# Kernel optimization log

Hardware: AMD Instinct MI355X
Metric: run time of the kernel (lower is better)

Reference implementation:

```python
import jax, jax.numpy as jnp
import numpy as np

GRID = (128, 128, 128)
CENTER = (0.0, 0.0, 0.0)
SIZE = (400.0, 400.0, 400.0)
KERNEL_WIDTH = float(np.sqrt(3.0 * 3.0 * np.pi))  # ~5.317 (from module source)
SIGMA = KERNEL_WIDTH / 2.0
W = 2  # transverse window half-width in voxels (kernel_width / voxel_size ~ 1.7)
ROTATIONS = {'x': [1, 2, 0], 'y': [0, 2, 1], 'z': [0, 1, 2]}
N_LORS = 200000


def _make_lors(key, n, axis, half):
    # endpoints: main-axis coords pinned to the two FOV faces, transverse uniform
    u = jax.random.uniform(key, (n, 6), minval=-half, maxval=half, dtype=jnp.float32)
    u = u.at[:, axis].set(-half).at[:, axis + 3].set(half)
    return u


def setup_inputs() -> dict:
    key = jax.random.key(0)
    k0, k1, k2, k3 = jax.random.split(key, 4)
    image = jax.random.uniform(k0, GRID, dtype=jnp.float32)
    half = SIZE[0] / 2.0
    return {
        'image': image,
        'xlors': _make_lors(k1, N_LORS, 0, half),
        'ylors': _make_lors(k2, N_LORS, 1, half),
        'zlors': _make_lors(k3, N_LORS, 2, half),
    }


def _project_axis(image, lors, perm):
    # rotate image / geometry so the LOR main axis is the last (slice) axis
    img = jnp.transpose(image, perm)                      # [gx, gy, gz]
    g = [GRID[i] for i in perm]
    c = [CENTER[i] for i in perm]
    s = [SIZE[i] for i in perm]
    dx, dy, dz = s[0] / g[0], s[1] / g[1], s[2] / g[2]
    xmin, ymin, zmin = c[0] - s[0] / 2, c[1] - s[1] / 2, c[2] - s[2] / 2

    p0 = lors[:, jnp.array(perm)]                          # [N,3]
    p1 = lors[:, jnp.array([i + 3 for i in perm])]         # [N,3]
    dvec = p1 - p0
    L = jnp.sqrt(jnp.sum(dvec * dvec, axis=1))             # LOR length
    dzl = dvec[:, 2]
    path = dz * L / jnp.abs(dzl)                           # path length per slice

    di = jnp.arange(-W, W + 1)
    doff = jnp.stack(jnp.meshgrid(di, di, indexing='ij'), -1).reshape(-1, 2)  # [25,2]

    def step(acc, k):
        zc = zmin + (k.astype(jnp.float32) + 0.5) * dz     # slice-plane center
        t = (zc - p0[:, 2]) / dzl                          # [N] line parameter
        xc = p0[:, 0] + t * dvec[:, 0]
        yc = p0[:, 1] + t * dvec[:, 1]
        i0 = jnp.floor((xc - xmin) / dx).astype(jnp.int32)
        j0 = jnp.floor((yc - ymin) / dy).astype(jnp.int32)
        ii = i0[:, None] + doff[None, :, 0]                # [N,25]
        jj = j0[:, None] + doff[None, :, 1]
        xi = xmin + (ii.astype(jnp.float32) + 0.5) * dx
        yj = ymin + (jj.astype(jnp.float32) + 0.5) * dy
        d2 = (xi - xc[:, None]) ** 2 + (yj - yc[:, None]) ** 2
        w = jnp.exp(-d2 / (2.0 * SIGMA * SIGMA))
        w = w * (d2 <= KERNEL_WIDTH * KERNEL_WIDTH).astype(jnp.float32)
        inb = ((ii >= 0) & (ii < g[0]) & (jj >= 0) & (jj < g[1])).astype(jnp.float32)
        valid = ((t >= 0.0) & (t <= 1.0)).astype(jnp.float32)
        sl = jax.lax.dynamic_index_in_dim(img, k, axis=2, keepdims=False)  # [gx,gy]
        vals = sl[jnp.clip(ii, 0, g[0] - 1), jnp.clip(jj, 0, g[1] - 1)]
        contrib = jnp.sum(w * inb * vals, axis=1) * path * valid
        return acc + contrib, None

    acc, _ = jax.lax.scan(step, jnp.zeros(lors.shape[0], jnp.float32), jnp.arange(g[2]))
    return acc


def reference(image, xlors, ylors, zlors):
    px = _project_axis(image, xlors, ROTATIONS['x'])
    py = _project_axis(image, ylors, ROTATIONS['y'])
    pz = _project_axis(image, zlors, ROTATIONS['z'])
    return jnp.stack([px, py, pz])  # [3, N]
```

## Files before the change

### kernel.cpp

```cpp
#include <hip/hip_runtime.h>
#include <math.h>

constexpr float DXC    = 3.125f;
constexpr float INV_DX = 0.32f;
constexpr float XMINC  = -200.0f;
constexpr float KW2    = 9.0f * 3.14159265358979323846f;
constexpr float DXC2   = DXC * DXC;
constexpr float KW2C   = KW2 / DXC2;
constexpr float NEGL2C = -(2.0f / KW2) * 1.4426950408889634f * DXC2;
constexpr float WOFF   = 1.7983f;

constexpr int TPB    = 1024;
constexpr int LPB    = 1024;
constexpr int KSPLIT = 4;
constexpr int KCH    = 128 / KSPLIT;
constexpr int QTAB   = 1024;

__device__ inline unsigned bf16_rn(float x) {
    unsigned u = __float_as_uint(x);
    return (u + 0x7fffu + ((u >> 16) & 1u)) >> 16;
}
__device__ inline unsigned pk_bf16(float x, float y) {
    return bf16_rn(x) | (bf16_rn(y) << 16);
}
__device__ inline float uaf(unsigned u) { return __uint_as_float(u); }

__global__ __launch_bounds__(256) void prep2_kernel(const float* __restrict__ img,
                                                    ushort* __restrict__ V0, ushort* __restrict__ V1,
                                                    ushort* __restrict__ V2, ushort* __restrict__ S0,
                                                    ushort* __restrict__ S1, ushort* __restrict__ S2) {
    int o = blockIdx.x * 256 + threadIdx.x;
    int c = o & 127, b = (o >> 7) & 127, a = o >> 14;
    float x  = img[o];
    float xn = (c < 127) ? img[o + 1] : 0.0f;
    unsigned h  = bf16_rn(x);
    unsigned hn = bf16_rn(xn);
    V0[o] = (ushort)h;
    S0[o] = (ushort)((c < 127) ? hn : 0u);
    int p1 = (b << 14) | (a << 7) | c;
    V1[p1] = (ushort)h;
    S1[p1] = (ushort)((c < 127) ? hn : 0u);
    V2[o] = (ushort)bf16_rn(img[(b << 14) | (c << 7) | a]);
    S2[o] = (ushort)((c < 127) ? bf16_rn(img[(b << 14) | ((c + 1) << 7) | a]) : 0u);
}

__global__ __launch_bounds__(256) void prep_kernel(const float* __restrict__ img,
                                                   ushort* __restrict__ V0,
                                                   ushort* __restrict__ V1,
                                                   ushort* __restrict__ V2) {
    int o = blockIdx.x * 256 + threadIdx.x;
    float x = img[o];
    unsigned h = bf16_rn(x);
    V0[o] = (ushort)h;
    int c = o & 127, b = (o >> 7) & 127, a = o >> 14;
    V1[(b << 14) | (a << 7) | c] = (ushort)h;
    int j = o & 127, i = (o >> 7) & 127, k = o >> 14;
    V2[o] = (ushort)bf16_rn(img[(i << 14) | (j << 7) | k]);
}

__global__ __launch_bounds__(1024) void zero_kernel(float* __restrict__ out, int m) {
    int i = blockIdx.x * 1024 + threadIdx.x;
    if (i < m) out[i] = 0.0f;
}

__device__ inline void stage_one(const ushort* __restrict__ V, int k, int tid, void* dst) {
    const char* src = (const char*)(V + ((size_t)k << 14));
    char* d = (char*)dst;
    int wbase = (tid >> 6) << 10;
    int lane16 = (tid & 63) << 4;
#pragma unroll
    for (int c = 0; c < 2; ++c) {
        int half = c << 14;
        __builtin_amdgcn_global_load_lds(
            (__attribute__((address_space(1))) void*)(const_cast<char*>(src + half + wbase + lane16)),
            (__attribute__((address_space(3))) void*)(d + half + wbase),
            16, 0, 0);
    }
}

struct WIN {
    float eb[4], ea[4], b[4], t[4];
    const uint* base;
    int adw;
};

__device__ inline WIN make_window(float u, float v, const uint2* wt,
                                  const uint* A, const uint* B) {
    WIN w;
    float e0f = fminf(fmaxf(floorf(v - WOFF), 0.0f), 124.0f);
    int   e0  = (int)e0f;
    int   qv  = min((int)((v - e0f) * (QTAB / 4.0f)), QTAB - 1);
    uint2 tb = wt[qv];
    w.eb[0] = uaf(tb.x << 16); w.eb[1] = uaf(tb.x & 0xffff0000u);
    w.eb[2] = uaf(tb.y << 16); w.eb[3] = uaf(tb.y & 0xffff0000u);
    float db0 = e0f + 0.5f - v;
    w.b[0] = db0 * db0;
    float gb = fmaf(2.0f, db0, 1.0f);
    w.b[1] = w.b[0] + gb; float gb1 = gb + 2.0f;
    w.b[2] = w.b[1] + gb1;
    w.b[3] = w.b[2] + gb1 + 2.0f;

    float i0f = fminf(fmaxf(floorf(u - WOFF), 0.0f), 124.0f);
    int   i0c = (int)i0f;
    int   qu  = min((int)((u - i0f) * (QTAB / 4.0f)), QTAB - 1);
    uint2 ta = wt[qu];
    w.ea[0] = uaf(ta.x << 16); w.ea[1] = uaf(ta.x & 0xffff0000u);
    w.ea[2] = uaf(ta.y << 16); w.ea[3] = uaf(ta.y & 0xffff0000u);
    float da0 = i0f + 0.5f - u;
    float a0 = da0 * da0;
    float ga = fmaf(2.0f, da0, 1.0f);
    float a1 = a0 + ga; float ga1 = ga + 2.0f;
    float a2 = a1 + ga1;
    float a3 = a2 + ga1 + 2.0f;
    w.t[0] = KW2C - a0; w.t[1] = KW2C - a1; w.t[2] = KW2C - a2; w.t[3] = KW2C - a3;

    w.base = (e0 & 1) ? B : A;
    w.adw  = (i0c << 6) + (e0 >> 1);
    return w;
}

template <int AXIS>
__device__ void proj_axis8(uint* slA, uint* slB, uint2* wt,
                           const ushort* __restrict__ V, const ushort* __restrict__ S,
                           const float* __restrict__ lors,
                           float* __restrict__ out, int n, int blk, int ks)
{
    const int tid = threadIdx.x;
    const int lor = blk * LPB + tid;
    const bool active = lor < n;
    const int lorc = active ? lor : n - 1;

    const float* l = lors + (size_t)lorc * 6;
    float l0 = l[0], l1 = l[1], l2 = l[2], l3 = l[3], l4 = l[4], l5 = l[5];
    float p0x, p0y, p0z, p1x, p1y, p1z;
    if (AXIS == 0)      { p0x = l1; p0y = l2; p0z = l0; p1x = l4; p1y = l5; p1z = l3; }
    else if (AXIS == 1) { p0x = l0; p0y = l2; p0z = l1; p1x = l3; p1y = l5; p1z = l4; }
    else                { p0x = l0; p0y = l1; p0z = l2; p1x = l3; p1y = l4; p1z = l5; }

    float dvx = p1x - p0x, dvy = p1y - p0y, dvz = p1z - p0z;
    float L     = sqrtf(dvx * dvx + dvy * dvy + dvz * dvz);
    float pathL = DXC * L / fabsf(dvz);
    float invdz = 1.0f / dvz;

    float dux  = dvx * INV_DX, ux0 = (p0x - XMINC) * INV_DX;
    float dvyS = dvy * INV_DX, vy0 = (p0y - XMINC) * INV_DX;
    float tzs = invdz, tz0 = -p0z * invdz;

    const int k0 = ks * KCH, k1 = k0 + KCH;
    float dt = DXC * tzs;
    float cu = dux * dt, cv = dvyS * dt;
    float zc0 = fmaf((float)k0, DXC, XMINC + 0.5f * DXC);
    float t0  = fmaf(zc0, tzs, tz0);
    float u   = fmaf(t0, dux, ux0);
    float v   = fmaf(t0, dvyS, vy0);
    float acc = 0.0f;

    stage_one(V, k0, tid, slA);
    stage_one(S, k0, tid, slB);
    {
        float s = ((float)tid + 0.5f) * (4.0f / (float)QTAB);
        float o0 = 0.5f - s, o1 = 1.5f - s, o2 = 2.5f - s, o3 = 3.5f - s;
        float e0 = exp2f(o0 * o0 * NEGL2C);
        float e1 = exp2f(o1 * o1 * NEGL2C);
        float e2 = exp2f(o2 * o2 * NEGL2C);
        float e3 = exp2f(o3 * o3 * NEGL2C);
        wt[tid] = make_uint2(pk_bf16(e0, e1), pk_bf16(e2, e3));
    }
    __syncthreads();

    WIN w = make_window(u, v, wt, slA, slB);

    for (int k = k0; k < k1; ++k) {
#pragma unroll
        for (int r = 0; r < 4; ++r) {
            uint d0 = w.base[w.adw + (r << 6)];
            uint d1 = w.base[w.adw + (r << 6) + 1];
            float w0 = uaf(d0 << 16);
            float w1 = uaf(d0 & 0xffff0000u);
            float w2 = uaf(d1 << 16);
            float w3 = uaf(d1 & 0xffff0000u);
            float tr = w.t[r];
            float rs;
            rs = __fmul_rn((w.b[0] <= tr) ? w.eb[0] : 0.0f, w0);
            rs = fmaf((w.b[1] <= tr) ? w.eb[1] : 0.0f, w1, rs);
            rs = fmaf((w.b[2] <= tr) ? w.eb[2] : 0.0f, w2, rs);
            rs = fmaf((w.b[3] <= tr) ? w.eb[3] : 0.0f, w3, rs);
            acc = fmaf(w.ea[r], rs, acc);
        }

        if (k < k1 - 1) {
            float un = u + cu, vn = v + cv;
            __syncthreads();
            stage_one(V, k + 1, tid, slA);
            stage_one(S, k + 1, tid, slB);
            w = make_window(un, vn, wt, slA, slB);
            u = un; v = vn;
            __syncthreads();
        }
    }

    if (active) atomicAdd(out + lor, acc * pathL);
}

__global__ __launch_bounds__(TPB, 8) void proj_fused8(const ushort* __restrict__ V0,
                                                      const ushort* __restrict__ V1,
                                                      const ushort* __restrict__ V2,
                                                      const ushort* __restrict__ S0,
                                                      const ushort* __restrict__ S1,
                                                      const ushort* __restrict__ S2,
                                                      const float* __restrict__ xl,
                                                      const float* __restrict__ yl,
                                                      const float* __restrict__ zl,
                                                      float* __restrict__ out,
                                                      int n, int nblk)
{
    __shared__ uint  slA[8192];
    __shared__ uint  slB[8192];
    __shared__ uint2 wt[QTAB];
    int per = nblk * KSPLIT;
    int axis = blockIdx.x / per;
    int r = blockIdx.x - axis * per;
    int blk = r >> 2;
    int ks  = r & 3;
    if (axis == 0)      proj_axis8<0>(slA, slB, wt, V0, S0, xl, out, n, blk, ks);
    else if (axis == 1) proj_axis8<1>(slA, slB, wt, V1, S1, yl, out + n, n, blk, ks);
    else                proj_axis8<2>(slA, slB, wt, V2, S2, zl, out + 2 * (size_t)n, n, blk, ks);
}

template <int AXIS>
__device__ inline void stage_issue(const float* __restrict__ img, int k, int tid,
                                   float4 st[4]) {
#pragma unroll
    for (int c = 0; c < 4; ++c) {
        int f4 = tid + TPB * c;
        int fl = f4 << 2;
        if (AXIS == 2) {
            int i = fl >> 7, j = fl & 127;
            const float* p = img + (i << 14) + (j << 7) + k;
            st[c] = make_float4(p[0], p[128], p[256], p[384]);
        } else {
            int off;
            if (AXIS == 1) off = ((fl >> 7) << 14) | (k << 7) | (fl & 127);
            else           off = (k << 14) | fl;
            st[c] = *reinterpret_cast<const float4*>(img + off);
        }
    }
}

__device__ inline void stage_write(const float4 st[4], ushort* slb, int tid) {
    uint* w = reinterpret_cast<uint*>(slb);
#pragma unroll
    for (int c = 0; c < 4; ++c) {
        int f4 = tid + TPB * c;
        w[f4 * 2]     = pk_bf16(st[c].x, st[c].y);
        w[f4 * 2 + 1] = pk_bf16(st[c].z, st[c].w);
    }
}

template <int AXIS, bool PRE>
__device__ void proj_axis7(ushort (*sl)[16384], float4* wtab,
                           const ushort* __restrict__ V,
                           const float*  __restrict__ imgF,
                           const float*  __restrict__ lors,
                           float* __restrict__ out, int n, int blk, int ks)
{
    const int tid = threadIdx.x;
    const int lor = blk * LPB + tid;
    const bool active = lor < n;
    const int lorc = active ? lor : n - 1;

    const float* l = lors + (size_t)lorc * 6;
    float l0 = l[0], l1 = l[1], l2 = l[2], l3 = l[3], l4 = l[4], l5 = l[5];
    float p0x, p0y, p0z, p1x, p1y, p1z;
    if (AXIS == 0)      { p0x = l1; p0y = l2; p0z = l0; p1x = l4; p1y = l5; p1z = l3; }
    else if (AXIS == 1) { p0x = l0; p0y = l2; p0z = l1; p1x = l3; p1y = l5; p1z = l4; }
    else                { p0x = l0; p0y = l1; p0z = l2; p1x = l3; p1y = l4; p1z = l5; }

    float dvx = p1x - p0x, dvy = p1y - p0y, dvz = p1z - p0z;
    float L     = sqrtf(dvx * dvx + dvy * dvy + dvz * dvz);
    float pathL = DXC * L / fabsf(dvz);
    float invdz = 1.0f / dvz;

    float dux  = dvx * INV_DX, ux0 = (p0x - XMINC) * INV_DX;
    float dvyS = dvy * INV_DX, vy0 = (p0y - XMINC) * INV_DX;
    float tzs = invdz, tz0 = -p0z * invdz;

    const int k0 = ks * KCH, k1 = k0 + KCH;
    float dt = DXC * tzs;
    float cu = dux * dt, cv = dvyS * dt;
    float zc0 = fmaf((float)k0, DXC, XMINC + 0.5f * DXC);
    float t0  = fmaf(zc0, tzs, tz0);
    float u   = fmaf(t0, dux, ux0);
    float v   = fmaf(t0, dvyS, vy0);
    float acc = 0.0f;

    if (PRE) {
        stage_one(V, k0, tid, sl[k0 & 1]);
    } else {
        float4 st[4];
        stage_issue<AXIS>(imgF, k0, tid, st);
        stage_write(st, sl[k0 & 1], tid);
    }
    {
        float s = ((float)tid + 0.5f) * (4.0f / (float)QTAB);
        float4 e;
        float o0 = 0.5f - s, o1 = 1.5f - s, o2 = 2.5f - s, o3 = 3.5f - s;
        e.x = exp2f(o0 * o0 * NEGL2C);
        e.y = exp2f(o1 * o1 * NEGL2C);
        e.z = exp2f(o2 * o2 * NEGL2C);
        e.w = exp2f(o3 * o3 * NEGL2C);
        wtab[tid] = e;
    }
    __syncthreads();

    for (int k = k0; k < k1; ++k) {
        const ushort* sbuf = sl[k & 1];
        float4 st2[4];
        if (k < k1 - 1) {
            if (PRE) stage_one(V, k + 1, tid, sl[(k & 1) ^ 1]);
            else     stage_issue<AXIS>(imgF, k + 1, tid, st2);
        }

        float e0f = fminf(fmaxf(floorf(v - WOFF), 0.0f), 124.0f);
        int   e0  = (int)e0f;
        int   qv  = min((int)((v - e0f) * (QTAB / 4.0f)), QTAB - 1);
        float4 eb = wtab[qv];
        float db0 = e0f + 0.5f - v;
        float b0 = db0 * db0;
        float gb = fmaf(2.0f, db0, 1.0f);
        float b1 = b0 + gb, gb1 = gb + 2.0f;
        float b2 = b1 + gb1, gb2 = gb1 + 2.0f;
        float b3 = b2 + gb2;

        float i0f = fminf(fmaxf(floorf(u - WOFF), 0.0f), 124.0f);
        int   i0c = (int)i0f;
        int   qu  = min((int)((u - i0f) * (QTAB / 4.0f)), QTAB - 1);
        float4 ea = wtab[qu];
        float da0 = i0f + 0.5f - u;
        float a0 = da0 * da0;
        float ga = fmaf(2.0f, da0, 1.0f);
        float a1 = a0 + ga, ga1 = ga + 2.0f;
        float a2 = a1 + ga1, ga2 = ga1 + 2.0f;
        float a3 = a2 + ga2;
        float thr[4] = {KW2C - a0, KW2C - a1, KW2C - a2, KW2C - a3};
        float eaa[4] = {ea.x, ea.y, ea.z, ea.w};

        const uint* s32 = reinterpret_cast<const uint*>(sbuf);
        int dwc = e0 >> 1;
        int sh  = (e0 & 1) << 4;
        int rowdw = (i0c << 6) + dwc;
#pragma unroll
        for (int r = 0; r < 4; ++r) {
            const uint* sr = s32 + rowdw + (r << 6);
            uint d0 = sr[0], d1 = sr[1], d2 = sr[2];
            uint p01 = __builtin_amdgcn_alignbit(d1, d0, sh);
            uint p23 = __builtin_amdgcn_alignbit(d2, d1, sh);
            float w0 = uaf(p01 << 16);
            float w1 = uaf(p01 & 0xffff0000u);
            float w2 = uaf(p23 << 16);
            float w3 = uaf(p23 & 0xffff0000u);
            float tr = thr[r];
            float rs;
            rs = __fmul_rn((b0 <= tr) ? eb.x : 0.0f, w0);
            rs = fmaf((b1 <= tr) ? eb.y : 0.0f, w1, rs);
            rs = fmaf((b2 <= tr) ? eb.z : 0.0f, w2, rs);
            rs = fmaf((b3 <= tr) ? eb.w : 0.0f, w3, rs);
            acc = fmaf(eaa[r], rs, acc);
        }

        u += cu; v += cv;

        if (k < k1 - 1) {
            if (!PRE) stage_write(st2, sl[(k & 1) ^ 1], tid);
            __syncthreads();
        }
    }

    if (active) atomicAdd(out + lor, acc * pathL);
}

template <bool PRE>
__global__ __launch_bounds__(TPB, 8) void proj_fused7(const float* __restrict__ img,
                                                      const ushort* __restrict__ V0,
                                                      const ushort* __restrict__ V1,
                                                      const ushort* __restrict__ V2,
                                                      const float* __restrict__ xl,
                                                      const float* __restrict__ yl,
                                                      const float* __restrict__ zl,
                                                      float* __restrict__ out,
                                                      int n, int nblk)
{
    __shared__ ushort sl[2][16384];
    __shared__ float4 wtab[QTAB];
    int per = nblk * KSPLIT;
    int axis = blockIdx.x / per;
    int r = blockIdx.x - axis * per;
    int blk = r >> 2;
    int ks  = r & 3;
    if (axis == 0)      proj_axis7<0, PRE>(sl, wtab, V0, img, xl, out, n, blk, ks);
    else if (axis == 1) proj_axis7<1, PRE>(sl, wtab, V1, img, yl, out + n, n, blk, ks);
    else                proj_axis7<2, PRE>(sl, wtab, V2, img, zl, out + 2 * (size_t)n, n, blk, ks);
}

extern "C" void kernel_launch(void* const* d_in, const int* in_sizes, int n_in,
                              void* d_out, int out_size, void* d_ws, size_t ws_size,
                              hipStream_t stream) {
    const float* img   = (const float*)d_in[0];
    const float* xlors = (const float*)d_in[1];
    const float* ylors = (const float*)d_in[2];
    const float* zlors = (const float*)d_in[3];
    float* out = (float*)d_out;

    int n = in_sizes[1] / 6;
    int nblk = (n + LPB - 1) / LPB;
    int m = 3 * n;

    zero_kernel<<<(m + 1023) / 1024, 1024, 0, stream>>>(out, m);

    constexpr size_t VOL = 128 * 128 * 128;
    int grid = 3 * nblk * KSPLIT;

    if (ws_size >= 6 * VOL * sizeof(ushort)) {
        ushort* V0 = (ushort*)d_ws;
        ushort* V1 = V0 + VOL;  ushort* V2 = V1 + VOL;
        ushort* S0 = V2 + VOL;  ushort* S1 = S0 + VOL;  ushort* S2 = S1 + VOL;
        prep2_kernel<<<VOL / 256, 256, 0, stream>>>(img, V0, V1, V2, S0, S1, S2);
        proj_fused8<<<grid, TPB, 0, stream>>>(V0, V1, V2, S0, S1, S2,
                                              xlors, ylors, zlors, out, n, nblk);
    } else if (ws_size >= 3 * VOL * sizeof(ushort)) {
        ushort* V0 = (ushort*)d_ws;
        ushort* V1 = V0 + VOL;  ushort* V2 = V1 + VOL;
        prep_kernel<<<VOL / 256, 256, 0, stream>>>(img, V0, V1, V2);
        proj_fused7<true><<<grid, TPB, 0, stream>>>(img, V0, V1, V2,
                                                    xlors, ylors, zlors, out, n, nblk);
    } else {
        proj_fused7<false><<<grid, TPB, 0, stream>>>(img, nullptr, nullptr, nullptr,
                                                     xlors, ylors, zlors, out, n, nblk);
    }
}
```

Before: 326.3 us.

## Process two LORs per thread per staged slice and replace the window mask with a weight threshold

```diff
diff --git a/kernel.cpp b/kernel.cpp
--- a/kernel.cpp
+++ b/kernel.cpp
@@ -9,10 +9,12 @@
 constexpr float KW2C   = KW2 / DXC2;
 constexpr float NEGL2C = -(2.0f / KW2) * 1.4426950408889634f * DXC2;
 constexpr float WOFF   = 1.7983f;
+constexpr float WMIN   = 0.13533528323661270f;
 
 constexpr int TPB    = 1024;
 constexpr int LPB    = 1024;
-constexpr int KSPLIT = 4;
+constexpr int LPT    = 2;
+constexpr int KSPLIT = 8;
 constexpr int KCH    = 128 / KSPLIT;
 constexpr int QTAB   = 1024;
 
@@ -78,131 +80,126 @@
     }
 }
 
-struct WIN {
-    float eb[4], ea[4], b[4], t[4];
-    const uint* base;
-    int adw;
-};
-
-__device__ inline WIN make_window(float u, float v, const uint2* wt,
-                                  const uint* A, const uint* B) {
-    WIN w;
-    float e0f = fminf(fmaxf(floorf(v - WOFF), 0.0f), 124.0f);
-    int   e0  = (int)e0f;
-    int   qv  = min((int)((v - e0f) * (QTAB / 4.0f)), QTAB - 1);
-    uint2 tb = wt[qv];
-    w.eb[0] = uaf(tb.x << 16); w.eb[1] = uaf(tb.x & 0xffff0000u);
-    w.eb[2] = uaf(tb.y << 16); w.eb[3] = uaf(tb.y & 0xffff0000u);
-    float db0 = e0f + 0.5f - v;
-    w.b[0] = db0 * db0;
-    float gb = fmaf(2.0f, db0, 1.0f);
-    w.b[1] = w.b[0] + gb; float gb1 = gb + 2.0f;
-    w.b[2] = w.b[1] + gb1;
-    w.b[3] = w.b[2] + gb1 + 2.0f;
-
-    float i0f = fminf(fmaxf(floorf(u - WOFF), 0.0f), 124.0f);
-    int   i0c = (int)i0f;
-    int   qu  = min((int)((u - i0f) * (QTAB / 4.0f)), QTAB - 1);
-    uint2 ta = wt[qu];
-    w.ea[0] = uaf(ta.x << 16); w.ea[1] = uaf(ta.x & 0xffff0000u);
-    w.ea[2] = uaf(ta.y << 16); w.ea[3] = uaf(ta.y & 0xffff0000u);
-    float da0 = i0f + 0.5f - u;
-    float a0 = da0 * da0;
-    float ga = fmaf(2.0f, da0, 1.0f);
-    float a1 = a0 + ga; float ga1 = ga + 2.0f;
-    float a2 = a1 + ga1;
-    float a3 = a2 + ga1 + 2.0f;
-    w.t[0] = KW2C - a0; w.t[1] = KW2C - a1; w.t[2] = KW2C - a2; w.t[3] = KW2C - a3;
-
-    w.base = (e0 & 1) ? B : A;
-    w.adw  = (i0c << 6) + (e0 >> 1);
-    return w;
-}
+struct WIN { float ea0, ea1, ea2, ea3, eb0, eb1, eb2, eb3; int adw; };
+struct LST { float u, v, cu, cv, path; };
 
 template <int AXIS>
-__device__ void proj_axis8(uint* slA, uint* slB, uint2* wt,
-                           const ushort* __restrict__ V, const ushort* __restrict__ S,
-                           const float* __restrict__ lors,
-                           float* __restrict__ out, int n, int blk, int ks)
-{
-    const int tid = threadIdx.x;
-    const int lor = blk * LPB + tid;
-    const bool active = lor < n;
-    const int lorc = active ? lor : n - 1;
-
+__device__ inline LST lor_setup(const float* __restrict__ lors, int lorc, int k0) {
     const float* l = lors + (size_t)lorc * 6;
     float l0 = l[0], l1 = l[1], l2 = l[2], l3 = l[3], l4 = l[4], l5 = l[5];
     float p0x, p0y, p0z, p1x, p1y, p1z;
     if (AXIS == 0)      { p0x = l1; p0y = l2; p0z = l0; p1x = l4; p1y = l5; p1z = l3; }
     else if (AXIS == 1) { p0x = l0; p0y = l2; p0z = l1; p1x = l3; p1y = l5; p1z = l4; }
     else                { p0x = l0; p0y = l1; p0z = l2; p1x = l3; p1y = l4; p1z = l5; }
-
     float dvx = p1x - p0x, dvy = p1y - p0y, dvz = p1z - p0z;
     float L     = sqrtf(dvx * dvx + dvy * dvy + dvz * dvz);
-    float pathL = DXC * L / fabsf(dvz);
     float invdz = 1.0f / dvz;
-
+    LST s;
+    s.path = DXC * L / fabsf(dvz);
     float dux  = dvx * INV_DX, ux0 = (p0x - XMINC) * INV_DX;
     float dvyS = dvy * INV_DX, vy0 = (p0y - XMINC) * INV_DX;
-    float tzs = invdz, tz0 = -p0z * invdz;
+    float tz0 = -p0z * invdz;
+    float dt = DXC * invdz;
+    s.cu = dux * dt; s.cv = dvyS * dt;
+    float zc0 = fmaf((float)k0, DXC, XMINC + 0.5f * DXC);
+    float t0  = fmaf(zc0, invdz, tz0);
+    s.u = fmaf(t0, dux, ux0);
+    s.v = fmaf(t0, dvyS, vy0);
+    return s;
+}
+
+__device__ inline WIN mkwin(float u, float v, const float4* wt) {
+    WIN w;
+    float e0f = fminf(fmaxf(floorf(v - WOFF), 0.0f), 124.0f);
+    float i0f = fminf(fmaxf(floorf(u - WOFF), 0.0f), 124.0f);
+    int qv = min((int)((v - e0f) * (QTAB / 4.0f)), QTAB - 1);
+    int qu = min((int)((u - i0f) * (QTAB / 4.0f)), QTAB - 1);
+    float4 eb = wt[qv];
+    float4 ea = wt[qu];
+    int e0 = (int)e0f, i0 = (int)i0f;
+    w.adw = (i0 << 6) + (e0 >> 1) + ((e0 & 1) << 13);
+    w.ea0 = ea.x; w.ea1 = ea.y; w.ea2 = ea.z; w.ea3 = ea.w;
+    w.eb0 = eb.x; w.eb1 = eb.y; w.eb2 = eb.z; w.eb3 = eb.w;
+    return w;
+}
+
+__device__ inline float do_slice(const WIN& w, const uint* __restrict__ sl, float acc) {
+#pragma unroll
+    for (int r = 0; r < 4; ++r) {
+        int a = w.adw + (r << 6);
+        uint d0 = sl[a], d1 = sl[a + 1];
+        float x0 = uaf(d0 << 16), x1 = uaf(d0 & 0xffff0000u);
+        float x2 = uaf(d1 << 16), x3 = uaf(d1 & 0xffff0000u);
+        float er = (r == 0) ? w.ea0 : (r == 1) ? w.ea1 : (r == 2) ? w.ea2 : w.ea3;
+        float p0 = er * w.eb0, p1 = er * w.eb1, p2 = er * w.eb2, p3 = er * w.eb3;
+        p0 = (p0 >= WMIN) ? p0 : 0.0f;
+        p1 = (p1 >= WMIN) ? p1 : 0.0f;
+        p2 = (p2 >= WMIN) ? p2 : 0.0f;
+        p3 = (p3 >= WMIN) ? p3 : 0.0f;
+        acc = fmaf(p0, x0, acc);
+        acc = fmaf(p1, x1, acc);
+        acc = fmaf(p2, x2, acc);
+        acc = fmaf(p3, x3, acc);
+    }
+    return acc;
+}
+
+template <int AXIS>
+__device__ void proj_axis9(uint* sl, float4* wt,
+                           const ushort* __restrict__ V, const ushort* __restrict__ S,
+                           const float* __restrict__ lors,
+                           float* __restrict__ out, int n, int blk, int ks)
+{
+    const int tid = threadIdx.x;
+    int lor0 = blk * (LPT * LPB) + tid;
+    int lor1 = lor0 + LPB;
+    bool act0 = lor0 < n, act1 = lor1 < n;
+    int lc0 = act0 ? lor0 : n - 1;
+    int lc1 = act1 ? lor1 : n - 1;
 
     const int k0 = ks * KCH, k1 = k0 + KCH;
-    float dt = DXC * tzs;
-    float cu = dux * dt, cv = dvyS * dt;
-    float zc0 = fmaf((float)k0, DXC, XMINC + 0.5f * DXC);
-    float t0  = fmaf(zc0, tzs, tz0);
-    float u   = fmaf(t0, dux, ux0);
-    float v   = fmaf(t0, dvyS, vy0);
-    float acc = 0.0f;
-
-    stage_one(V, k0, tid, slA);
-    stage_one(S, k0, tid, slB);
+    LST s0 = lor_setup<AXIS>(lors, lc0, k0);
+    LST s1 = lor_setup<AXIS>(lors, lc1, k0);
+    float acc0 = 0.0f, acc1 = 0.0f;
+
+    stage_one(V, k0, tid, sl);
+    stage_one(S, k0, tid, sl + 8192);
     {
         float s = ((float)tid + 0.5f) * (4.0f / (float)QTAB);
+        float4 e;
         float o0 = 0.5f - s, o1 = 1.5f - s, o2 = 2.5f - s, o3 = 3.5f - s;
-        float e0 = exp2f(o0 * o0 * NEGL2C);
-        float e1 = exp2f(o1 * o1 * NEGL2C);
-        float e2 = exp2f(o2 * o2 * NEGL2C);
-        float e3 = exp2f(o3 * o3 * NEGL2C);
-        wt[tid] = make_uint2(pk_bf16(e0, e1), pk_bf16(e2, e3));
+        e.x = exp2f(o0 * o0 * NEGL2C);
+        e.y = exp2f(o1 * o1 * NEGL2C);
+        e.z = exp2f(o2 * o2 * NEGL2C);
+        e.w = exp2f(o3 * o3 * NEGL2C);
+        wt[tid] = e;
     }
     __syncthreads();
 
-    WIN w = make_window(u, v, wt, slA, slB);
+    WIN w0 = mkwin(s0.u, s0.v, wt);
+    WIN w1 = mkwin(s1.u, s1.v, wt);
 
     for (int k = k0; k < k1; ++k) {
-#pragma unroll
-        for (int r = 0; r < 4; ++r) {
-            uint d0 = w.base[w.adw + (r << 6)];
-            uint d1 = w.base[w.adw + (r << 6) + 1];
-            float w0 = uaf(d0 << 16);
-            float w1 = uaf(d0 & 0xffff0000u);
-            float w2 = uaf(d1 << 16);
-            float w3 = uaf(d1 & 0xffff0000u);
-            float tr = w.t[r];
-            float rs;
-            rs = __fmul_rn((w.b[0] <= tr) ? w.eb[0] : 0.0f, w0);
-            rs = fmaf((w.b[1] <= tr) ? w.eb[1] : 0.0f, w1, rs);
-            rs = fmaf((w.b[2] <= tr) ? w.eb[2] : 0.0f, w2, rs);
-            rs = fmaf((w.b[3] <= tr) ? w.eb[3] : 0.0f, w3, rs);
-            acc = fmaf(w.ea[r], rs, acc);
-        }
+        acc0 = do_slice(w0, sl, acc0);
+        acc1 = do_slice(w1, sl, acc1);
 
         if (k < k1 - 1) {
-            float un = u + cu, vn = v + cv;
+            s0.u += s0.cu; s0.v += s0.cv;
+            s1.u += s1.cu; s1.v += s1.cv;
             __syncthreads();
-            stage_one(V, k + 1, tid, slA);
-            stage_one(S, k + 1, tid, slB);
-            w = make_window(un, vn, wt, slA, slB);
-            u = un; v = vn;
+            stage_one(V, k + 1, tid, sl);
+            stage_one(S, k + 1, tid, sl + 8192);
+            w0 = mkwin(s0.u, s0.v, wt);
+            w1 = mkwin(s1.u, s1.v, wt);
             __syncthreads();
         }
     }
 
-    if (active) atomicAdd(out + lor, acc * pathL);
-}
-
-__global__ __launch_bounds__(TPB, 8) void proj_fused8(const ushort* __restrict__ V0,
+    if (act0) atomicAdd(out + lor0, acc0 * s0.path);
+    if (act1) atomicAdd(out + lor1, acc1 * s1.path);
+}
+
+__global__ __launch_bounds__(TPB, 2) void proj_fused9(const ushort* __restrict__ V0,
                                                       const ushort* __restrict__ V1,
                                                       const ushort* __restrict__ V2,
                                                       const ushort* __restrict__ S0,
@@ -214,17 +211,16 @@
                                                       float* __restrict__ out,
                                                       int n, int nblk)
 {
-    __shared__ uint  slA[8192];
-    __shared__ uint  slB[8192];
-    __shared__ uint2 wt[QTAB];
+    __shared__ uint   sl[16384];
+    __shared__ float4 wt[QTAB];
     int per = nblk * KSPLIT;
     int axis = blockIdx.x / per;
     int r = blockIdx.x - axis * per;
-    int blk = r >> 2;
-    int ks  = r & 3;
-    if (axis == 0)      proj_axis8<0>(slA, slB, wt, V0, S0, xl, out, n, blk, ks);
-    else if (axis == 1) proj_axis8<1>(slA, slB, wt, V1, S1, yl, out + n, n, blk, ks);
-    else                proj_axis8<2>(slA, slB, wt, V2, S2, zl, out + 2 * (size_t)n, n, blk, ks);
+    int blk = r >> 3;
+    int ks  = r & 7;
+    if (axis == 0)      proj_axis9<0>(sl, wt, V0, S0, xl, out, n, blk, ks);
+    else if (axis == 1) proj_axis9<1>(sl, wt, V1, S1, yl, out + n, n, blk, ks);
+    else                proj_axis9<2>(sl, wt, V2, S2, zl, out + 2 * (size_t)n, n, blk, ks);
 }
 
 template <int AXIS>
@@ -269,29 +265,9 @@
     const bool active = lor < n;
     const int lorc = active ? lor : n - 1;
 
-    const float* l = lors + (size_t)lorc * 6;
-    float l0 = l[0], l1 = l[1], l2 = l[2], l3 = l[3], l4 = l[4], l5 = l[5];
-    float p0x, p0y, p0z, p1x, p1y, p1z;
-    if (AXIS == 0)      { p0x = l1; p0y = l2; p0z = l0; p1x = l4; p1y = l5; p1z = l3; }
-    else if (AXIS == 1) { p0x = l0; p0y = l2; p0z = l1; p1x = l3; p1y = l5; p1z = l4; }
-    else                { p0x = l0; p0y = l1; p0z = l2; p1x = l3; p1y = l4; p1z = l5; }
-
-    float dvx = p1x - p0x, dvy = p1y - p0y, dvz = p1z - p0z;
-    float L     = sqrtf(dvx * dvx + dvy * dvy + dvz * dvz);
-    float pathL = DXC * L / fabsf(dvz);
-    float invdz = 1.0f / dvz;
-
-    float dux  = dvx * INV_DX, ux0 = (p0x - XMINC) * INV_DX;
-    float dvyS = dvy * INV_DX, vy0 = (p0y - XMINC) * INV_DX;
-    float tzs = invdz, tz0 = -p0z * invdz;
-
     const int k0 = ks * KCH, k1 = k0 + KCH;
-    float dt = DXC * tzs;
-    float cu = dux * dt, cv = dvyS * dt;
-    float zc0 = fmaf((float)k0, DXC, XMINC + 0.5f * DXC);
-    float t0  = fmaf(zc0, tzs, tz0);
-    float u   = fmaf(t0, dux, ux0);
-    float v   = fmaf(t0, dvyS, vy0);
+    LST s = lor_setup<AXIS>(lors, lorc, k0);
+    float u = s.u, v = s.v, cu = s.cu, cv = s.cv;
     float acc = 0.0f;
 
     if (PRE) {
@@ -302,9 +278,9 @@
         stage_write(st, sl[k0 & 1], tid);
     }
     {
-        float s = ((float)tid + 0.5f) * (4.0f / (float)QTAB);
+        float sx = ((float)tid + 0.5f) * (4.0f / (float)QTAB);
         float4 e;
-        float o0 = 0.5f - s, o1 = 1.5f - s, o2 = 2.5f - s, o3 = 3.5f - s;
+        float o0 = 0.5f - sx, o1 = 1.5f - sx, o2 = 2.5f - sx, o3 = 3.5f - sx;
         e.x = exp2f(o0 * o0 * NEGL2C);
         e.y = exp2f(o1 * o1 * NEGL2C);
         e.z = exp2f(o2 * o2 * NEGL2C);
@@ -325,24 +301,10 @@
         int   e0  = (int)e0f;
         int   qv  = min((int)((v - e0f) * (QTAB / 4.0f)), QTAB - 1);
         float4 eb = wtab[qv];
-        float db0 = e0f + 0.5f - v;
-        float b0 = db0 * db0;
-        float gb = fmaf(2.0f, db0, 1.0f);
-        float b1 = b0 + gb, gb1 = gb + 2.0f;
-        float b2 = b1 + gb1, gb2 = gb1 + 2.0f;
-        float b3 = b2 + gb2;
-
         float i0f = fminf(fmaxf(floorf(u - WOFF), 0.0f), 124.0f);
         int   i0c = (int)i0f;
         int   qu  = min((int)((u - i0f) * (QTAB / 4.0f)), QTAB - 1);
         float4 ea = wtab[qu];
-        float da0 = i0f + 0.5f - u;
-        float a0 = da0 * da0;
-        float ga = fmaf(2.0f, da0, 1.0f);
-        float a1 = a0 + ga, ga1 = ga + 2.0f;
-        float a2 = a1 + ga1, ga2 = ga1 + 2.0f;
-        float a3 = a2 + ga2;
-        float thr[4] = {KW2C - a0, KW2C - a1, KW2C - a2, KW2C - a3};
         float eaa[4] = {ea.x, ea.y, ea.z, ea.w};
 
         const uint* s32 = reinterpret_cast<const uint*>(sbuf);
@@ -355,17 +317,20 @@
             uint d0 = sr[0], d1 = sr[1], d2 = sr[2];
             uint p01 = __builtin_amdgcn_alignbit(d1, d0, sh);
             uint p23 = __builtin_amdgcn_alignbit(d2, d1, sh);
-            float w0 = uaf(p01 << 16);
-            float w1 = uaf(p01 & 0xffff0000u);
-            float w2 = uaf(p23 << 16);
-            float w3 = uaf(p23 & 0xffff0000u);
-            float tr = thr[r];
-            float rs;
-            rs = __fmul_rn((b0 <= tr) ? eb.x : 0.0f, w0);
-            rs = fmaf((b1 <= tr) ? eb.y : 0.0f, w1, rs);
-            rs = fmaf((b2 <= tr) ? eb.z : 0.0f, w2, rs);
-            rs = fmaf((b3 <= tr) ? eb.w : 0.0f, w3, rs);
-            acc = fmaf(eaa[r], rs, acc);
+            float x0 = uaf(p01 << 16);
+            float x1 = uaf(p01 & 0xffff0000u);
+            float x2 = uaf(p23 << 16);
+            float x3 = uaf(p23 & 0xffff0000u);
+            float er = eaa[r];
+            float p0 = er * eb.x, p1 = er * eb.y, p2 = er * eb.z, p3 = er * eb.w;
+            p0 = (p0 >= WMIN) ? p0 : 0.0f;
+            p1 = (p1 >= WMIN) ? p1 : 0.0f;
+            p2 = (p2 >= WMIN) ? p2 : 0.0f;
+            p3 = (p3 >= WMIN) ? p3 : 0.0f;
+            acc = fmaf(p0, x0, acc);
+            acc = fmaf(p1, x1, acc);
+            acc = fmaf(p2, x2, acc);
+            acc = fmaf(p3, x3, acc);
         }
 
         u += cu; v += cv;
@@ -376,11 +341,11 @@
         }
     }
 
-    if (active) atomicAdd(out + lor, acc * pathL);
+    if (active) atomicAdd(out + lor, acc * s.path);
 }
 
 template <bool PRE>
-__global__ __launch_bounds__(TPB, 8) void proj_fused7(const float* __restrict__ img,
+__global__ __launch_bounds__(TPB, 2) void proj_fused7(const float* __restrict__ img,
                                                       const ushort* __restrict__ V0,
                                                       const ushort* __restrict__ V1,
                                                       const ushort* __restrict__ V2,
@@ -395,8 +360,8 @@
     int per = nblk * KSPLIT;
     int axis = blockIdx.x / per;
     int r = blockIdx.x - axis * per;
-    int blk = r >> 2;
-    int ks  = r & 3;
+    int blk = r >> 3;
+    int ks  = r & 7;
     if (axis == 0)      proj_axis7<0, PRE>(sl, wtab, V0, img, xl, out, n, blk, ks);
     else if (axis == 1) proj_axis7<1, PRE>(sl, wtab, V1, img, yl, out + n, n, blk, ks);
     else                proj_axis7<2, PRE>(sl, wtab, V2, img, zl, out + 2 * (size_t)n, n, blk, ks);
@@ -412,28 +377,32 @@
     float* out = (float*)d_out;
 
     int n = in_sizes[1] / 6;
-    int nblk = (n + LPB - 1) / LPB;
     int m = 3 * n;
 
     zero_kernel<<<(m + 1023) / 1024, 1024, 0, stream>>>(out, m);
 
     constexpr size_t VOL = 128 * 128 * 128;
-    int grid = 3 * nblk * KSPLIT;
 
     if (ws_size >= 6 * VOL * sizeof(ushort)) {
+        int nblk = (n + LPT * LPB - 1) / (LPT * LPB);
+        int grid = 3 * nblk * KSPLIT;
         ushort* V0 = (ushort*)d_ws;
         ushort* V1 = V0 + VOL;  ushort* V2 = V1 + VOL;
         ushort* S0 = V2 + VOL;  ushort* S1 = S0 + VOL;  ushort* S2 = S1 + VOL;
         prep2_kernel<<<VOL / 256, 256, 0, stream>>>(img, V0, V1, V2, S0, S1, S2);
-        proj_fused8<<<grid, TPB, 0, stream>>>(V0, V1, V2, S0, S1, S2,
+        proj_fused9<<<grid, TPB, 0, stream>>>(V0, V1, V2, S0, S1, S2,
                                               xlors, ylors, zlors, out, n, nblk);
     } else if (ws_size >= 3 * VOL * sizeof(ushort)) {
+        int nblk = (n + LPB - 1) / LPB;
+        int grid = 3 * nblk * KSPLIT;
         ushort* V0 = (ushort*)d_ws;
         ushort* V1 = V0 + VOL;  ushort* V2 = V1 + VOL;
         prep_kernel<<<VOL / 256, 256, 0, stream>>>(img, V0, V1, V2);
         proj_fused7<true><<<grid, TPB, 0, stream>>>(img, V0, V1, V2,
                                                     xlors, ylors, zlors, out, n, nblk);
     } else {
+        int nblk = (n + LPB - 1) / LPB;
+        int grid = 3 * nblk * KSPLIT;
         proj_fused7<false><<<grid, TPB, 0, stream>>>(img, nullptr, nullptr, nullptr,
                                                      xlors, ylors, zlors, out, n, nblk);
     }
```

After: 359.9 us. 10.3% more time.
